# Performance work log

Measured on AMD Instinct MI355X. Metric: run time of the kernel, lower is better.

## Reference

```python
import jax, jax.numpy as jnp
import numpy as np

# Black-oil PINO constants (from init_kwargs)
UIR = 5000.0; PINI_ALT = 1000.0
LUB = 0.1; HUB = 1.0; AAY = 50.0; BBY = 500.0
SWI = 0.1; SWR = 0.1; UW = 1.0; BW = 1.0; UO = 2.5; BO = 1.1
MAXZ = 6000.0
NX = 128; NY = 128; NZ = 4
B = 8; T = 10


def _pad_edge(x, axis):
    pw = [(0, 0)] * x.ndim
    pw[axis] = (1, 1)
    return jnp.pad(x, pw, mode='edge')


def d1(x, axis, h):
    # central difference [-0.5, 0, 0.5]/h with replicate padding (modulus-sym dx, order=1)
    xp = _pad_edge(x, axis)
    n = xp.shape[axis]
    f = jax.lax.slice_in_dim(xp, 2, n, axis=axis)
    b = jax.lax.slice_in_dim(xp, 0, n - 2, axis=axis)
    return (f - b) * (0.5 / h)


def d2(x, axis, h):
    # second derivative [1, -2, 1]/h^2 with replicate padding (modulus-sym ddx, order=1)
    xp = _pad_edge(x, axis)
    n = xp.shape[axis]
    f = jax.lax.slice_in_dim(xp, 2, n, axis=axis)
    c = jax.lax.slice_in_dim(xp, 1, n - 1, axis=axis)
    b = jax.lax.slice_in_dim(xp, 0, n - 2, axis=axis)
    return (f - 2.0 * c + b) / (h * h)


def setup_inputs() -> dict:
    key = jax.random.key(0)
    ks = jax.random.split(key, 9)
    shp = (B, T, NZ, NX, NY)
    return {
        'pressure': jax.random.uniform(ks[0], shp, jnp.float32),
        'perm': jax.random.uniform(ks[1], shp, jnp.float32),
        'Q': jax.random.normal(ks[2], shp, jnp.float32),
        'Qw': jax.random.normal(ks[3], shp, jnp.float32),
        'Time': jax.random.uniform(ks[4], shp, jnp.float32, minval=0.05, maxval=1.0),
        'Pini': jax.random.uniform(ks[5], shp, jnp.float32),
        'Phi': jax.random.uniform(ks[6], shp, jnp.float32),
        'Swini': jax.random.uniform(ks[7], shp, jnp.float32),
        'water_sat': jax.random.uniform(ks[8], shp, jnp.float32),
    }


def reference(pressure, perm, Q, Qw, Time, Pini, Phi, Swini, water_sat):
    # fields are [B, T, nz, nx, ny]; axis 3 == nx ('dim=0'), axis 4 == ny ('dim=1')
    u = pressure * PINI_ALT
    fin = Q * UIR
    finwater = Qw * UIR
    dta = Time * MAXZ
    dxf = 1.0 / u.shape[3]
    siniuse = Swini[0, 0, 0, 0, 0]

    # rescale permeability from [LUB, HUB] to [AAY, BBY]
    m = (BBY - AAY) / (HUB - LUB)
    a = m * perm + (AAY - m * LUB)

    sat = water_sat
    # prior saturation: sini at t=0, shifted sat afterwards
    prior_sat = jnp.concatenate(
        [jnp.broadcast_to(siniuse, sat[:, :1].shape).astype(sat.dtype), sat[:, :-1]], axis=1)
    dsw = jnp.clip(sat - prior_sat, 0.001, None)

    S = (prior_sat - SWI) / (1.0 - SWI - SWR)
    Mw = jnp.square(S) / (UW * BW)
    Mo = jnp.square(1.0 - S) / (UO * BO)
    a1 = (Mw + Mo) * a        # total mobility * perm
    a1water = Mw * a          # water mobility * perm

    # pressure derivatives (all timesteps)
    dudx = d1(u, 3, dxf)
    dudy = d1(u, 4, dxf)
    dduddx = d2(u, 3, dxf)
    dduddy = d2(u, 4, dxf)

    # mobility-field derivatives: torch code passes channel=0, i.e. only time index 0,
    # then vstack-replicates across the T time channels -> broadcast over axis 1
    dcdx = jnp.broadcast_to(d1(a1[:, :1], 3, dxf), a1.shape)
    dcdy = jnp.broadcast_to(d1(a1[:, :1], 4, dxf), a1.shape)
    dadx = jnp.broadcast_to(d1(a1water[:, :1], 3, dxf), a1.shape)
    dady = jnp.broadcast_to(d1(a1water[:, :1], 4, dxf), a1.shape)

    p_loss = dxf * 1e-05 * (fin + dcdx * dudx + a1 * dduddx + dcdy * dudy + a1 * dduddy)
    flux = dadx * dudx + a1water * dduddx + dady * dudy + a1water * dduddy
    s_loss = dxf * 1e-05 * (Phi * (dsw / dta) - (flux + finwater))
    return p_loss, s_loss
```

## Files before the change

### kernel.cpp

```cpp
#include <hip/hip_runtime.h>

#define NXC 128
#define NYC 128
#define NZC 4
#define BC  8
#define TC  10

#define TSTRIDE 65536
#define NTOT    5242880
#define NQUAD   1310720
#define HALFQ   655360

typedef float vf4 __attribute__((ext_vector_type(4)));

__global__ __launch_bounds__(256) void blackoil_kernel(
    const float* __restrict__ pressure,
    const float* __restrict__ perm,
    const float* __restrict__ Q,
    const float* __restrict__ Qw,
    const float* __restrict__ Time_,
    const float* __restrict__ Phi,
    const float* __restrict__ Swini,
    const float* __restrict__ wsat,
    float* __restrict__ out)
{
    const int gid = blockIdx.x * blockDim.x + threadIdx.x;

    const float sini = Swini[0];

    int   base_[2];
    vf4 pc_[2], pxm_[2], pxp_[2];
    float pym_[2], pyp_[2];
    vf4 k0c_[2], k0m_[2], k0p_[2];
    float kym_[2], kyp_[2];
    vf4 kc_[2], sat_[2], pri_[2], qv_[2], qwv_[2], tv_[2], phv_[2];
    int   t_[2];

#pragma unroll
    for (int k = 0; k < 2; ++k) {
        const int gq   = gid + k * HALFQ;
        const int base = gq << 2;
        base_[k] = base;

        const int y = base & (NYC - 1);
        const int x = (base >> 7) & (NXC - 1);
        const int t = (base >> 16) % TC;
        t_[k] = t;

        const int xm  = (x > 0)        ? -NYC : 0;
        const int xp  = (x < NXC - 1)  ?  NYC : 0;
        const int ymo = (y > 0)        ? -1   : 0;
        const int ypo = (y < NYC - 4)  ?  4   : 3;

        pc_ [k] = *(const vf4*)(pressure + base);
        pxm_[k] = *(const vf4*)(pressure + base + xm);
        pxp_[k] = *(const vf4*)(pressure + base + xp);
        pym_[k] = pressure[base + ymo];
        pyp_[k] = pressure[base + ypo];

        const int i0 = base - t * TSTRIDE;
        k0c_[k] = *(const vf4*)(perm + i0);
        k0m_[k] = *(const vf4*)(perm + i0 + xm);
        k0p_[k] = *(const vf4*)(perm + i0 + xp);
        kym_[k] = perm[i0 + ymo];
        kyp_[k] = perm[i0 + ypo];

        kc_ [k] = *(const vf4*)(perm + base);
        sat_[k] = *(const vf4*)(wsat + base);
        const int ip = base - ((t > 0) ? TSTRIDE : 0);
        pri_[k] = *(const vf4*)(wsat + ip);

        qv_ [k] = *(const vf4*)(Q     + base);
        qwv_[k] = *(const vf4*)(Qw    + base);
        tv_ [k] = *(const vf4*)(Time_ + base);
        phv_[k] = *(const vf4*)(Phi   + base);
    }

    __builtin_amdgcn_sched_barrier(0);

    const float S0 = (sini - 0.1f) * 1.25f;
    const float cw = S0 * S0;
    const float ct = cw + (1.0f - S0) * (1.0f - S0) * (1.0f / 2.75f);
    const float scale = 7.8125e-8f;
    const float DK = 32000.0f;

#pragma unroll
    for (int k = 0; k < 2; ++k) {
        const int base = base_[k];
        vf4 pri = pri_[k];
        if (t_[k] == 0) { pri = (vf4){sini, sini, sini, sini}; }

        const float ucA [4] = { pc_[k].x,  pc_[k].y,  pc_[k].z,  pc_[k].w  };
        const float uxmA[4] = { pxm_[k].x, pxm_[k].y, pxm_[k].z, pxm_[k].w };
        const float uxpA[4] = { pxp_[k].x, pxp_[k].y, pxp_[k].z, pxp_[k].w };
        const float uymA[4] = { pym_[k],   pc_[k].x,  pc_[k].y,  pc_[k].z  };
        const float uypA[4] = { pc_[k].y,  pc_[k].z,  pc_[k].w,  pyp_[k]   };

        const float k0mA[4] = { k0m_[k].x, k0m_[k].y, k0m_[k].z, k0m_[k].w };
        const float k0pA[4] = { k0p_[k].x, k0p_[k].y, k0p_[k].z, k0p_[k].w };
        const float kymA[4] = { kym_[k],   k0c_[k].x, k0c_[k].y, k0c_[k].z };
        const float kypA[4] = { k0c_[k].y, k0c_[k].z, k0c_[k].w, kyp_[k]   };

        const float kcA [4] = { kc_[k].x,  kc_[k].y,  kc_[k].z,  kc_[k].w  };
        const float saA [4] = { sat_[k].x, sat_[k].y, sat_[k].z, sat_[k].w };
        const float prA [4] = { pri.x,     pri.y,     pri.z,     pri.w     };
        const float qA  [4] = { qv_[k].x,  qv_[k].y,  qv_[k].z,  qv_[k].w  };
        const float qwA [4] = { qwv_[k].x, qwv_[k].y, qwv_[k].z, qwv_[k].w };
        const float tmA [4] = { tv_[k].x,  tv_[k].y,  tv_[k].z,  tv_[k].w  };
        const float phA [4] = { phv_[k].x, phv_[k].y, phv_[k].z, phv_[k].w };

        float pl[4], sl[4];
#pragma unroll
        for (int j = 0; j < 4; ++j) {
            const float uc   = ucA[j]  * 1000.0f;
            const float uxm2 = uxmA[j] * 1000.0f;
            const float uxp2 = uxpA[j] * 1000.0f;
            const float uym2 = uymA[j] * 1000.0f;
            const float uyp2 = uypA[j] * 1000.0f;

            const float dudx   = (uxp2 - uxm2) * 64.0f;
            const float dudy   = (uyp2 - uym2) * 64.0f;
            const float dduddx = (uxp2 - 2.0f * uc + uxm2) * 16384.0f;
            const float dduddy = (uyp2 - 2.0f * uc + uym2) * 16384.0f;

            const float dpx = (k0pA[j] - k0mA[j]) * DK;
            const float dpy = (kypA[j] - kymA[j]) * DK;
            const float g1  = dpx * dudx + dpy * dudy;
            const float lap = dduddx + dduddy;

            const float a   = 500.0f * kcA[j];
            const float dsw = fmaxf(saA[j] - prA[j], 0.001f);
            const float S   = (prA[j] - 0.1f) * 1.25f;
            const float Mw  = S * S;
            const float Mo  = (1.0f - S) * (1.0f - S) * (1.0f / 2.75f);
            const float a1  = (Mw + Mo) * a;
            const float a1w = Mw * a;

            pl[j] = scale * (qA[j] * 5000.0f + ct * g1 + a1 * lap);
            const float flux = cw * g1 + a1w * lap;
            sl[j] = scale * (phA[j] * (dsw / (tmA[j] * 6000.0f)) - (flux + qwA[j] * 5000.0f));
        }

        vf4 po = { pl[0], pl[1], pl[2], pl[3] };
        vf4 so = { sl[0], sl[1], sl[2], sl[3] };
        __builtin_nontemporal_store(po, (vf4*)(out + base));
        __builtin_nontemporal_store(so, (vf4*)(out + base + NTOT));
    }
}

extern "C" void kernel_launch(void* const* d_in, const int* in_sizes, int n_in,
                              void* d_out, int out_size, void* d_ws, size_t ws_size,
                              hipStream_t stream) {
    const float* pressure = (const float*)d_in[0];
    const float* perm     = (const float*)d_in[1];
    const float* Q        = (const float*)d_in[2];
    const float* Qw       = (const float*)d_in[3];
    const float* Time_    = (const float*)d_in[4];
    const float* Phi      = (const float*)d_in[6];
    const float* Swini    = (const float*)d_in[7];
    const float* wsat     = (const float*)d_in[8];
    float* out = (float*)d_out;

    const int threads = 256;
    const int blocks  = HALFQ / threads;
    blackoil_kernel<<<blocks, threads, 0, stream>>>(
        pressure, perm, Q, Qw, Time_, Phi, Swini, wsat, out);
}
```

Before: 203.4 us.

## Switch to one scalar element per thread with nontemporal input loads

Replaces the 2x float4-per-thread scheme with one element per thread, launching 8x more threads. The streaming inputs (Q, Qw, Time, Phi) are now read with nontemporal loads. This removes the per-thread register pressure and the scheduling barrier, and relies on many more waves in flight to hide latency. The cost is scalar 4-byte memory accesses in place of 16-byte vector accesses, more neighbour loads per element, and more index arithmetic overall.

```diff
diff --git a/kernel.cpp b/kernel.cpp
--- a/kernel.cpp
+++ b/kernel.cpp
@@ -8,10 +8,6 @@
 
 #define TSTRIDE 65536
 #define NTOT    5242880
-#define NQUAD   1310720
-#define HALFQ   655360
-
-typedef float vf4 __attribute__((ext_vector_type(4)));
 
 __global__ __launch_bounds__(256) void blackoil_kernel(
     const float* __restrict__ pressure,
@@ -28,55 +24,37 @@
 
     const float sini = Swini[0];
 
-    int   base_[2];
-    vf4 pc_[2], pxm_[2], pxp_[2];
-    float pym_[2], pyp_[2];
-    vf4 k0c_[2], k0m_[2], k0p_[2];
-    float kym_[2], kyp_[2];
-    vf4 kc_[2], sat_[2], pri_[2], qv_[2], qwv_[2], tv_[2], phv_[2];
-    int   t_[2];
+    const int y = gid & (NYC - 1);
+    const int x = (gid >> 7) & (NXC - 1);
+    const int t = (gid >> 16) % TC;
 
-#pragma unroll
-    for (int k = 0; k < 2; ++k) {
-        const int gq   = gid + k * HALFQ;
-        const int base = gq << 2;
-        base_[k] = base;
+    const int xm = (x > 0)       ? -NYC : 0;
+    const int xp = (x < NXC - 1) ?  NYC : 0;
+    const int ym = (y > 0)       ? -1   : 0;
+    const int yp = (y < NYC - 1) ?  1   : 0;
 
-        const int y = base & (NYC - 1);
-        const int x = (base >> 7) & (NXC - 1);
-        const int t = (base >> 16) % TC;
-        t_[k] = t;
+    const float pc  = pressure[gid];
+    const float pxm = pressure[gid + xm];
+    const float pxp = pressure[gid + xp];
+    const float pym = pressure[gid + ym];
+    const float pyp = pressure[gid + yp];
 
-        const int xm  = (x > 0)        ? -NYC : 0;
-        const int xp  = (x < NXC - 1)  ?  NYC : 0;
-        const int ymo = (y > 0)        ? -1   : 0;
-        const int ypo = (y < NYC - 4)  ?  4   : 3;
+    const int i0 = gid - t * TSTRIDE;
+    const float k0xm = perm[i0 + xm];
+    const float k0xp = perm[i0 + xp];
+    const float k0ym = perm[i0 + ym];
+    const float k0yp = perm[i0 + yp];
 
-        pc_ [k] = *(const vf4*)(pressure + base);
-        pxm_[k] = *(const vf4*)(pressure + base + xm);
-        pxp_[k] = *(const vf4*)(pressure + base + xp);
-        pym_[k] = pressure[base + ymo];
-        pyp_[k] = pressure[base + ypo];
+    const float kc = perm[gid];
+    const float sa = wsat[gid];
+    const float prload = wsat[gid - ((t > 0) ? TSTRIDE : 0)];
 
-        const int i0 = base - t * TSTRIDE;
-        k0c_[k] = *(const vf4*)(perm + i0);
-        k0m_[k] = *(const vf4*)(perm + i0 + xm);
-        k0p_[k] = *(const vf4*)(perm + i0 + xp);
-        kym_[k] = perm[i0 + ymo];
-        kyp_[k] = perm[i0 + ypo];
+    const float q  = __builtin_nontemporal_load(Q     + gid);
+    const float qw = __builtin_nontemporal_load(Qw    + gid);
+    const float tm = __builtin_nontemporal_load(Time_ + gid);
+    const float ph = __builtin_nontemporal_load(Phi   + gid);
 
-        kc_ [k] = *(const vf4*)(perm + base);
-        sat_[k] = *(const vf4*)(wsat + base);
-        const int ip = base - ((t > 0) ? TSTRIDE : 0);
-        pri_[k] = *(const vf4*)(wsat + ip);
-
-        qv_ [k] = *(const vf4*)(Q     + base);
-        qwv_[k] = *(const vf4*)(Qw    + base);
-        tv_ [k] = *(const vf4*)(Time_ + base);
-        phv_[k] = *(const vf4*)(Phi   + base);
-    }
-
-    __builtin_amdgcn_sched_barrier(0);
+    const float pr = (t == 0) ? sini : prload;
 
     const float S0 = (sini - 0.1f) * 1.25f;
     const float cw = S0 * S0;
@@ -84,68 +62,36 @@
     const float scale = 7.8125e-8f;
     const float DK = 32000.0f;
 
-#pragma unroll
-    for (int k = 0; k < 2; ++k) {
-        const int base = base_[k];
-        vf4 pri = pri_[k];
-        if (t_[k] == 0) { pri = (vf4){sini, sini, sini, sini}; }
+    const float uc   = pc  * 1000.0f;
+    const float uxm2 = pxm * 1000.0f;
+    const float uxp2 = pxp * 1000.0f;
+    const float uym2 = pym * 1000.0f;
+    const float uyp2 = pyp * 1000.0f;
 
-        const float ucA [4] = { pc_[k].x,  pc_[k].y,  pc_[k].z,  pc_[k].w  };
-        const float uxmA[4] = { pxm_[k].x, pxm_[k].y, pxm_[k].z, pxm_[k].w };
-        const float uxpA[4] = { pxp_[k].x, pxp_[k].y, pxp_[k].z, pxp_[k].w };
-        const float uymA[4] = { pym_[k],   pc_[k].x,  pc_[k].y,  pc_[k].z  };
-        const float uypA[4] = { pc_[k].y,  pc_[k].z,  pc_[k].w,  pyp_[k]   };
+    const float dudx   = (uxp2 - uxm2) * 64.0f;
+    const float dudy   = (uyp2 - uym2) * 64.0f;
+    const float dduddx = (uxp2 - 2.0f * uc + uxm2) * 16384.0f;
+    const float dduddy = (uyp2 - 2.0f * uc + uym2) * 16384.0f;
 
-        const float k0mA[4] = { k0m_[k].x, k0m_[k].y, k0m_[k].z, k0m_[k].w };
-        const float k0pA[4] = { k0p_[k].x, k0p_[k].y, k0p_[k].z, k0p_[k].w };
-        const float kymA[4] = { kym_[k],   k0c_[k].x, k0c_[k].y, k0c_[k].z };
-        const float kypA[4] = { k0c_[k].y, k0c_[k].z, k0c_[k].w, kyp_[k]   };
+    const float dpx = (k0xp - k0xm) * DK;
+    const float dpy = (k0yp - k0ym) * DK;
+    const float g1  = dpx * dudx + dpy * dudy;
+    const float lap = dduddx + dduddy;
 
-        const float kcA [4] = { kc_[k].x,  kc_[k].y,  kc_[k].z,  kc_[k].w  };
-        const float saA [4] = { sat_[k].x, sat_[k].y, sat_[k].z, sat_[k].w };
-        const float prA [4] = { pri.x,     pri.y,     pri.z,     pri.w     };
-        const float qA  [4] = { qv_[k].x,  qv_[k].y,  qv_[k].z,  qv_[k].w  };
-        const float qwA [4] = { qwv_[k].x, qwv_[k].y, qwv_[k].z, qwv_[k].w };
-        const float tmA [4] = { tv_[k].x,  tv_[k].y,  tv_[k].z,  tv_[k].w  };
-        const float phA [4] = { phv_[k].x, phv_[k].y, phv_[k].z, phv_[k].w };
+    const float a   = 500.0f * kc;
+    const float dsw = fmaxf(sa - pr, 0.001f);
+    const float S   = (pr - 0.1f) * 1.25f;
+    const float Mw  = S * S;
+    const float Mo  = (1.0f - S) * (1.0f - S) * (1.0f / 2.75f);
+    const float a1  = (Mw + Mo) * a;
+    const float a1w = Mw * a;
 
-        float pl[4], sl[4];
-#pragma unroll
-        for (int j = 0; j < 4; ++j) {
-            const float uc   = ucA[j]  * 1000.0f;
-            const float uxm2 = uxmA[j] * 1000.0f;
-            const float uxp2 = uxpA[j] * 1000.0f;
-            const float uym2 = uymA[j] * 1000.0f;
-            const float uyp2 = uypA[j] * 1000.0f;
+    const float pl = scale * (q * 5000.0f + ct * g1 + a1 * lap);
+    const float flux = cw * g1 + a1w * lap;
+    const float sl = scale * (ph * (dsw / (tm * 6000.0f)) - (flux + qw * 5000.0f));
 
-            const float dudx   = (uxp2 - uxm2) * 64.0f;
-            const float dudy   = (uyp2 - uym2) * 64.0f;
-            const float dduddx = (uxp2 - 2.0f * uc + uxm2) * 16384.0f;
-            const float dduddy = (uyp2 - 2.0f * uc + uym2) * 16384.0f;
-
-            const float dpx = (k0pA[j] - k0mA[j]) * DK;
-            const float dpy = (kypA[j] - kymA[j]) * DK;
-            const float g1  = dpx * dudx + dpy * dudy;
-            const float lap = dduddx + dduddy;
-
-            const float a   = 500.0f * kcA[j];
-            const float dsw = fmaxf(saA[j] - prA[j], 0.001f);
-            const float S   = (prA[j] - 0.1f) * 1.25f;
-            const float Mw  = S * S;
-            const float Mo  = (1.0f - S) * (1.0f - S) * (1.0f / 2.75f);
-            const float a1  = (Mw + Mo) * a;
-            const float a1w = Mw * a;
-
-            pl[j] = scale * (qA[j] * 5000.0f + ct * g1 + a1 * lap);
-            const float flux = cw * g1 + a1w * lap;
-            sl[j] = scale * (phA[j] * (dsw / (tmA[j] * 6000.0f)) - (flux + qwA[j] * 5000.0f));
-        }
-
-        vf4 po = { pl[0], pl[1], pl[2], pl[3] };
-        vf4 so = { sl[0], sl[1], sl[2], sl[3] };
-        __builtin_nontemporal_store(po, (vf4*)(out + base));
-        __builtin_nontemporal_store(so, (vf4*)(out + base + NTOT));
-    }
+    __builtin_nontemporal_store(pl, out + gid);
+    __builtin_nontemporal_store(sl, out + gid + NTOT);
 }
 
 extern "C" void kernel_launch(void* const* d_in, const int* in_sizes, int n_in,
@@ -162,7 +108,7 @@
     float* out = (float*)d_out;
 
     const int threads = 256;
-    const int blocks  = HALFQ / threads;
+    const int blocks  = NTOT / threads;
     blackoil_kernel<<<blocks, threads, 0, stream>>>(
         pressure, perm, Q, Qw, Time_, Phi, Swini, wsat, out);
 }
```

Measured after the change: 192.0 us. -5.6%, faster.
